# Kernel tuning notes

Measured on AMD Instinct MI355X. Metric: run time of the kernel, lower is better.

## Reference

```python
import jax, jax.numpy as jnp
import numpy as np

HEADS = 8
DIM_HEAD = 64
INNER = HEADS * DIM_HEAD  # 512
QUERY_DIM = 1024
CONTEXT_DIM = 768
OUT_DIM = 1024


def setup_inputs() -> dict:
    key = jax.random.key(0)
    ks = jax.random.split(key, 7)
    B, Nq, Nk = 2, 4096, 4096
    s = 0.02
    return {
        "x": jax.random.normal(ks[0], (B, Nq, QUERY_DIM), dtype=jnp.float32),
        "context": jax.random.normal(ks[1], (B, Nk, CONTEXT_DIM), dtype=jnp.float32),
        "w_q": jax.random.normal(ks[2], (QUERY_DIM, INNER), dtype=jnp.float32) * s,
        "w_k": jax.random.normal(ks[3], (CONTEXT_DIM, INNER), dtype=jnp.float32) * s,
        "w_v": jax.random.normal(ks[4], (CONTEXT_DIM, INNER), dtype=jnp.float32) * s,
        "w_out": jax.random.normal(ks[5], (INNER, OUT_DIM), dtype=jnp.float32) * s,
        "b_out": jax.random.normal(ks[6], (OUT_DIM,), dtype=jnp.float32) * s,
    }


def reference(x, context, w_q, w_k, w_v, w_out, b_out):
    h, d = HEADS, DIM_HEAD
    scale = d ** (-0.5)
    B, Nq, _ = x.shape
    Nk = context.shape[1]
    # projections (no bias)
    q = x @ w_q            # [B, Nq, h*d]
    k = context @ w_k      # [B, Nk, h*d]
    v = context @ w_v      # [B, Nk, h*d]
    # split heads: b n (h d) -> b h n d
    q = q.reshape(B, Nq, h, d).transpose(0, 2, 1, 3)
    k = k.reshape(B, Nk, h, d).transpose(0, 2, 1, 3)
    v = v.reshape(B, Nk, h, d).transpose(0, 2, 1, 3)
    sim = jnp.einsum('bhid,bhjd->bhij', q, k) * scale  # [B, h, Nq, Nk]
    attn = jax.nn.softmax(sim, axis=-1)
    out = jnp.einsum('bhij,bhjd->bhid', attn, v)       # [B, h, Nq, d]
    out = out.transpose(0, 2, 1, 3).reshape(B, Nq, h * d)
    return out @ w_out + b_out  # dropout p=0 -> identity
```

## Files before the change

### kernel.cpp

```cpp
#include <hip/hip_runtime.h>
#include <hip/hip_bf16.h>
#include <stdint.h>

#define HEADS 8
#define DHEAD 64
#define INNER 512
#define QDIM 1024
#define CDIM 768
#define ODIM 1024
#define BATCH 2
#define NQ 4096
#define NKEY 4096

using bf16x8 = __attribute__((ext_vector_type(8))) short;
using f32x4  = __attribute__((ext_vector_type(4))) float;

__device__ __forceinline__ unsigned short f2bf(float x) {
    union { float f; unsigned u; } v; v.f = x;
    unsigned r = v.u + 0x7fffu + ((v.u >> 16) & 1u);
    return (unsigned short)(r >> 16);
}

__device__ __forceinline__ unsigned cvtpk(float a, float b) {
    unsigned r;
    asm("v_cvt_pk_bf16_f32 %0, %1, %2" : "=v"(r) : "v"(a), "v"(b));
    return r;
}

__device__ __forceinline__ float exp2a(float x) {
    float r;
    asm("v_exp_f32 %0, %1" : "=v"(r) : "v"(x));
    return r;
}

typedef const __attribute__((address_space(1))) unsigned int* gptr_t;
typedef __attribute__((address_space(3))) unsigned int* lptr_t;

__device__ __forceinline__ void async16(const void* g, void* l) {
    __builtin_amdgcn_global_load_lds((gptr_t)g, (lptr_t)l, 16, 0, 0);
}

#define SGB __builtin_amdgcn_sched_group_barrier

__global__ void k_convert(const float* __restrict__ in, unsigned short* __restrict__ out, int n4) {
    int i = blockIdx.x * blockDim.x + threadIdx.x;
    int stride = gridDim.x * blockDim.x;
    for (; i < n4; i += stride) {
        float4 v = reinterpret_cast<const float4*>(in)[i];
        ushort4 o;
        o.x = f2bf(v.x); o.y = f2bf(v.y); o.z = f2bf(v.z); o.w = f2bf(v.w);
        reinterpret_cast<ushort4*>(out)[i] = o;
    }
}

__global__ void k_transpose_bf16(const float* __restrict__ in, unsigned short* __restrict__ out,
                                 int R, int C) {
    __shared__ float tile[32][33];
    int c0 = blockIdx.x * 32, r0 = blockIdx.y * 32;
    int tx = threadIdx.x, ty = threadIdx.y;
    #pragma unroll
    for (int i = 0; i < 32; i += 8)
        tile[ty + i][tx] = in[(size_t)(r0 + ty + i) * C + c0 + tx];
    __syncthreads();
    #pragma unroll
    for (int i = 0; i < 32; i += 8)
        out[(size_t)(c0 + ty + i) * R + r0 + tx] = f2bf(tile[tx][ty + i]);
}

template <int OUTMODE>
__global__ __launch_bounds__(256) void k_gemm(const unsigned short* __restrict__ A,
                                              const unsigned short* __restrict__ BT,
                                              void* __restrict__ Cout,
                                              const float* __restrict__ bias,
                                              int M, int N, int Kd, float scale) {
    __shared__ alignas(16) unsigned short As[2][128 * 64];
    __shared__ alignas(16) unsigned short Bs[2][64 * 64];
    const int tid = threadIdx.x, lane = tid & 63, w = tid >> 6;
    const int g = lane >> 4, ql = lane & 15;
    const int m0 = blockIdx.x * 128, n0 = blockIdx.y * 64;
    const int wm = (w >> 1) * 64, wn = (w & 1) * 32;
    f32x4 acc[4][2] = {};

    const int srow = tid >> 3;
    const int schunk = ((tid & 7) ^ (srow & 7)) << 3;
    const unsigned short* gA = A + (size_t)(m0 + srow) * Kd + schunk;
    const unsigned short* gB = BT + (size_t)(n0 + srow) * Kd + schunk;

    auto stage = [&](int buf, int kt) {
        char* lA = (char*)As[buf] + (w << 10);
        char* lB = (char*)Bs[buf] + (w << 10);
        async16(gA + kt, lA);
        async16(gA + kt + (size_t)32 * Kd, lA + 4096);
        async16(gA + kt + (size_t)64 * Kd, lA + 8192);
        async16(gA + kt + (size_t)96 * Kd, lA + 12288);
        async16(gB + kt, lB);
        async16(gB + kt + (size_t)32 * Kd, lB + 4096);
    };

#define GCOMP(BUF) { \
        _Pragma("unroll") \
        for (int kk = 0; kk < 2; kk++) { \
            bf16x8 af[4], bfr[2]; \
            _Pragma("unroll") \
            for (int mi = 0; mi < 4; mi++) { \
                int r = wm + mi * 16 + ql; \
                af[mi] = *(const bf16x8*)((const char*)As[BUF] + r * 128 + ((kk * 64 + (g << 4)) ^ ((r & 7) << 4))); \
            } \
            _Pragma("unroll") \
            for (int ni = 0; ni < 2; ni++) { \
                int r = wn + ni * 16 + ql; \
                bfr[ni] = *(const bf16x8*)((const char*)Bs[BUF] + r * 128 + ((kk * 64 + (g << 4)) ^ ((r & 7) << 4))); \
            } \
            _Pragma("unroll") \
            for (int mi = 0; mi < 4; mi++) \
                _Pragma("unroll") \
                for (int ni = 0; ni < 2; ni++) \
                    acc[mi][ni] = __builtin_amdgcn_mfma_f32_16x16x32_bf16(af[mi], bfr[ni], acc[mi][ni], 0, 0, 0); \
        } \
    }

    stage(0, 0);
    for (int kt = 0; kt < Kd; kt += 128) {
        asm volatile("s_waitcnt vmcnt(0)" ::: "memory");
        __builtin_amdgcn_s_barrier();
        __builtin_amdgcn_sched_barrier(0);
        if (kt + 64 < Kd) stage(1, kt + 64);
        GCOMP(0);
        asm volatile("s_waitcnt vmcnt(0)" ::: "memory");
        __builtin_amdgcn_s_barrier();
        __builtin_amdgcn_sched_barrier(0);
        if (kt + 128 < Kd) stage(0, kt + 128);
        GCOMP(1);
    }
#undef GCOMP

    #pragma unroll
    for (int mi = 0; mi < 4; mi++) {
        #pragma unroll
        for (int ni = 0; ni < 2; ni++) {
            int col = n0 + wn + ni * 16 + ql;
            #pragma unroll
            for (int j = 0; j < 4; j++) {
                int row = m0 + wm + mi * 16 + (g << 2) + j;
                float v = acc[mi][ni][j] * scale;
                if (OUTMODE == 0) {
                    ((unsigned short*)Cout)[(size_t)row * N + col] = f2bf(v);
                } else {
                    ((float*)Cout)[(size_t)row * N + col] = v + bias[col];
                }
            }
        }
    }
}

__global__ __launch_bounds__(256, 2) void k_attn(const unsigned short* __restrict__ Q,
                                                 const unsigned short* __restrict__ K,
                                                 const unsigned short* __restrict__ Vt,
                                                 unsigned short* __restrict__ O) {
    __shared__ alignas(16) unsigned short Ks[2][64 * 64];
    __shared__ alignas(16) unsigned short Vs[2][64 * 64];
    const int tid = threadIdx.x, lane = tid & 63, w = tid >> 6;
    const int g = lane >> 4, ql = lane & 15;
    const int q0 = blockIdx.x * 128;
    const int b = blockIdx.y >> 3, h = blockIdx.y & 7;

    const unsigned short* qp = Q + (size_t)(b * NQ + q0 + w * 32 + ql) * INNER
                                 + h * DHEAD + (g << 3);
    bf16x8 qf00 = *(const bf16x8*)qp;
    bf16x8 qf01 = *(const bf16x8*)(qp + 32);
    bf16x8 qf10 = *(const bf16x8*)(qp + 16 * INNER);
    bf16x8 qf11 = *(const bf16x8*)(qp + 16 * INNER + 32);

    f32x4 po0[4] = {}, po1[4] = {};
    float ls0 = 0.f, ls1 = 0.f;
    const f32x4 zero4 = {0.f, 0.f, 0.f, 0.f};

    const int m0 = tid >> 3;
    const int rho0 = ((m0 & 28) << 1) + (m0 & 3);
    const int srcslot = ((tid & 7) ^ (m0 & 7)) << 3;
    const unsigned short* gK = K + (size_t)(b * NKEY + rho0) * INNER + h * DHEAD + srcslot;
    const unsigned short* gV = Vt + (size_t)(h * DHEAD + m0) * (BATCH * NKEY) + b * NKEY + srcslot;

    auto stageK = [&](int nb, int kt) {
        char* lK = (char*)Ks[nb] + (w << 10);
        async16(gK + (size_t)kt * INNER, lK);
        async16(gK + (size_t)(kt + 4) * INNER, lK + 4096);
    };
    auto stageV = [&](int nb, int kt) {
        char* lV = (char*)Vs[nb] + (w << 10);
        async16(gV + kt, lV);
        async16(gV + kt + (size_t)32 * (BATCH * NKEY), lV + 4096);
    };

    union pfu { bf16x8 v; unsigned u[4]; };

#define SMCHUNK(MI, SC0, SC1, pA, pB, lsa, lsb) { \
        float a0 = exp2a(SC0[MI][0]), a1 = exp2a(SC0[MI][1]); \
        float a2 = exp2a(SC0[MI][2]), a3 = exp2a(SC0[MI][3]); \
        float b0 = exp2a(SC1[MI][0]), b1 = exp2a(SC1[MI][1]); \
        float b2 = exp2a(SC1[MI][2]), b3 = exp2a(SC1[MI][3]); \
        lsa += (a0 + a1) + (a2 + a3); \
        lsb += (b0 + b1) + (b2 + b3); \
        pA[MI & 1].u[(MI >> 1) * 2 + 0] = cvtpk(a0, a1); \
        pA[MI & 1].u[(MI >> 1) * 2 + 1] = cvtpk(a2, a3); \
        pB[MI & 1].u[(MI >> 1) * 2 + 0] = cvtpk(b0, b1); \
        pB[MI & 1].u[(MI >> 1) * 2 + 1] = cvtpk(b2, b3); \
    }

#define QKM(KBUF, S0, S1) { \
        const char* Kb_ = (const char*)(KBUF); \
        _Pragma("unroll") \
        for (int mi = 0; mi < 4; mi++) { \
            int rK = mi * 16 + ql; \
            int sw = (rK & 7) << 4; \
            bf16x8 kf0 = *(const bf16x8*)(Kb_ + rK * 128 + ((g << 4) ^ sw)); \
            bf16x8 kf1 = *(const bf16x8*)(Kb_ + rK * 128 + ((64 + (g << 4)) ^ sw)); \
            S0[mi] = __builtin_amdgcn_mfma_f32_16x16x32_bf16(kf0, qf00, zero4, 0, 0, 0); \
            S0[mi] = __builtin_amdgcn_mfma_f32_16x16x32_bf16(kf1, qf01, S0[mi], 0, 0, 0); \
            S1[mi] = __builtin_amdgcn_mfma_f32_16x16x32_bf16(kf0, qf10, zero4, 0, 0, 0); \
            S1[mi] = __builtin_amdgcn_mfma_f32_16x16x32_bf16(kf1, qf11, S1[mi], 0, 0, 0); \
        } \
    }

#define PVM(VBUF, pA, pB) { \
        const char* Vb_ = (const char*)(VBUF); \
        bf16x8 vf0[4], vf1[4]; \
        _Pragma("unroll") \
        for (int mi = 0; mi < 4; mi++) { \
            int rV = mi * 16 + ql; \
            int sw = (rV & 7) << 4; \
            vf0[mi] = *(const bf16x8*)(Vb_ + rV * 128 + ((g << 4) ^ sw)); \
            vf1[mi] = *(const bf16x8*)(Vb_ + rV * 128 + ((64 + (g << 4)) ^ sw)); \
        } \
        _Pragma("unroll") \
        for (int mi = 0; mi < 4; mi++) { \
            po0[mi] = __builtin_amdgcn_mfma_f32_16x16x32_bf16(vf0[mi], pA[0].v, po0[mi], 0, 0, 0); \
            po0[mi] = __builtin_amdgcn_mfma_f32_16x16x32_bf16(vf1[mi], pA[1].v, po0[mi], 0, 0, 0); \
            po1[mi] = __builtin_amdgcn_mfma_f32_16x16x32_bf16(vf0[mi], pB[0].v, po1[mi], 0, 0, 0); \
            po1[mi] = __builtin_amdgcn_mfma_f32_16x16x32_bf16(vf1[mi], pB[1].v, po1[mi], 0, 0, 0); \
        } \
    }

#define ABODY(T, CUR, SC0, SC1, SN0, SN1, DO_K, DO_V) { \
        asm volatile("s_waitcnt vmcnt(0)" ::: "memory"); \
        __builtin_amdgcn_s_barrier(); \
        __builtin_amdgcn_sched_barrier(0); \
        if (DO_K) stageK(CUR, (T + 2) * 64); \
        if (DO_V) stageV(CUR ^ 1, (T + 1) * 64); \
        const char* Kb_ = (const char*)Ks[CUR ^ 1]; \
        bf16x8 kf0[4], kf1[4]; \
        _Pragma("unroll") \
        for (int mi = 0; mi < 4; mi++) { \
            int rK = mi * 16 + ql; \
            int sw = (rK & 7) << 4; \
            kf0[mi] = *(const bf16x8*)(Kb_ + rK * 128 + ((g << 4) ^ sw)); \
            kf1[mi] = *(const bf16x8*)(Kb_ + rK * 128 + ((64 + (g << 4)) ^ sw)); \
        } \
        __builtin_amdgcn_sched_group_barrier(0x100, 8, 0); \
        pfu pA[2], pB[2]; \
        float lsa = 0.f, lsb = 0.f; \
        _Pragma("unroll") \
        for (int mi = 0; mi < 4; mi++) { \
            SMCHUNK(mi, SC0, SC1, pA, pB, lsa, lsb); \
            __builtin_amdgcn_sched_group_barrier(0x2, 18, 0); \
            SN0[mi] = __builtin_amdgcn_mfma_f32_16x16x32_bf16(kf0[mi], qf00, zero4, 0, 0, 0); \
            SN0[mi] = __builtin_amdgcn_mfma_f32_16x16x32_bf16(kf1[mi], qf01, SN0[mi], 0, 0, 0); \
            SN1[mi] = __builtin_amdgcn_mfma_f32_16x16x32_bf16(kf0[mi], qf10, zero4, 0, 0, 0); \
            SN1[mi] = __builtin_amdgcn_mfma_f32_16x16x32_bf16(kf1[mi], qf11, SN1[mi], 0, 0, 0); \
            __builtin_amdgcn_sched_group_barrier(0x8, 4, 0); \
        } \
        ls0 += lsa; ls1 += lsb; \
        __builtin_amdgcn_s_setprio(1); \
        PVM(Vs[CUR], pA, pB); \
        __builtin_amdgcn_sched_group_barrier(0x100, 8, 0); \
        __builtin_amdgcn_sched_group_barrier(0x8, 16, 0); \
        __builtin_amdgcn_s_setprio(0); \
    }

    f32x4 sE0[4], sE1[4], sO0[4], sO1[4];

    stageK(0, 0); stageV(0, 0); stageK(1, 64);
    asm volatile("s_waitcnt vmcnt(2)" ::: "memory");
    __builtin_amdgcn_s_barrier();
    __builtin_amdgcn_sched_barrier(0);
    QKM(Ks[0], sE0, sE1);

    for (int t = 0; t < 62; t += 2) {
        ABODY(t, 0, sE0, sE1, sO0, sO1, 1, 1);
        ABODY(t + 1, 1, sO0, sO1, sE0, sE1, 1, 1);
    }
    ABODY(62, 0, sE0, sE1, sO0, sO1, 0, 1);

    asm volatile("s_waitcnt vmcnt(0)" ::: "memory");
    __builtin_amdgcn_s_barrier();
    __builtin_amdgcn_sched_barrier(0);
    {
        pfu pA[2], pB[2];
        float lsa = 0.f, lsb = 0.f;
        #pragma unroll
        for (int mi = 0; mi < 4; mi++) {
            SMCHUNK(mi, sO0, sO1, pA, pB, lsa, lsb);
        }
        ls0 += lsa; ls1 += lsb;
        PVM(Vs[1], pA, pB);
    }

    ls0 += __shfl_xor(ls0, 16); ls0 += __shfl_xor(ls0, 32);
    ls1 += __shfl_xor(ls1, 16); ls1 += __shfl_xor(ls1, 32);
    float inv0 = 1.0f / ls0, inv1 = 1.0f / ls1;
    unsigned short* op = O + (size_t)(b * NQ + q0 + w * 32 + ql) * INNER + h * DHEAD + (g << 2);
    #pragma unroll
    for (int mi = 0; mi < 4; mi++) {
        uint2 uu;
        uu.x = cvtpk(po0[mi][0] * inv0, po0[mi][1] * inv0);
        uu.y = cvtpk(po0[mi][2] * inv0, po0[mi][3] * inv0);
        *(uint2*)(op + mi * 16) = uu;
        uint2 vv;
        vv.x = cvtpk(po1[mi][0] * inv1, po1[mi][1] * inv1);
        vv.y = cvtpk(po1[mi][2] * inv1, po1[mi][3] * inv1);
        *(uint2*)(op + 16 * INNER + mi * 16) = vv;
    }
#undef ABODY
#undef PVM
#undef QKM
#undef SMCHUNK
}

extern "C" void kernel_launch(void* const* d_in, const int* in_sizes, int n_in,
                              void* d_out, int out_size, void* d_ws, size_t ws_size,
                              hipStream_t stream) {
    const float* x     = (const float*)d_in[0];
    const float* ctx   = (const float*)d_in[1];
    const float* w_q   = (const float*)d_in[2];
    const float* w_k   = (const float*)d_in[3];
    const float* w_v   = (const float*)d_in[4];
    const float* w_out = (const float*)d_in[5];
    const float* b_out = (const float*)d_in[6];
    float* out = (float*)d_out;

    char* ws = (char*)d_ws;
    size_t off = 0;
    auto alloc = [&](size_t bytes) { void* p = ws + off; off += (bytes + 255) & ~(size_t)255; return p; };
    unsigned short* xb  = (unsigned short*)alloc((size_t)BATCH * NQ * QDIM * 2);
    unsigned short* cb  = (unsigned short*)alloc((size_t)BATCH * NKEY * CDIM * 2);
    unsigned short* wqT = (unsigned short*)alloc((size_t)INNER * QDIM * 2);
    unsigned short* wkT = (unsigned short*)alloc((size_t)INNER * CDIM * 2);
    unsigned short* wvT = (unsigned short*)alloc((size_t)INNER * CDIM * 2);
    unsigned short* woT = (unsigned short*)alloc((size_t)ODIM * INNER * 2);
    unsigned short* Qb  = (unsigned short*)alloc((size_t)BATCH * NQ * INNER * 2);
    unsigned short* Kb  = (unsigned short*)alloc((size_t)BATCH * NKEY * INNER * 2);
    unsigned short* Vtb = (unsigned short*)alloc((size_t)INNER * BATCH * NKEY * 2);
    unsigned short* Ob  = (unsigned short*)alloc((size_t)BATCH * NQ * INNER * 2);

    k_convert<<<2048, 256, 0, stream>>>(x, xb, BATCH * NQ * QDIM / 4);
    k_convert<<<2048, 256, 0, stream>>>(ctx, cb, BATCH * NKEY * CDIM / 4);

    dim3 tb(32, 8);
    k_transpose_bf16<<<dim3(INNER / 32, QDIM / 32), tb, 0, stream>>>(w_q, wqT, QDIM, INNER);
    k_transpose_bf16<<<dim3(INNER / 32, CDIM / 32), tb, 0, stream>>>(w_k, wkT, CDIM, INNER);
    k_transpose_bf16<<<dim3(INNER / 32, CDIM / 32), tb, 0, stream>>>(w_v, wvT, CDIM, INNER);
    k_transpose_bf16<<<dim3(ODIM / 32, INNER / 32), tb, 0, stream>>>(w_out, woT, INNER, ODIM);

    k_gemm<0><<<dim3(8192 / 128, 512 / 64), 256, 0, stream>>>(xb, wqT, Qb, nullptr, 8192, 512, 1024, 0.1803368801111204f);
    k_gemm<0><<<dim3(8192 / 128, 512 / 64), 256, 0, stream>>>(cb, wkT, Kb, nullptr, 8192, 512, 768, 1.0f);
    k_gemm<0><<<dim3(512 / 128, 8192 / 64), 256, 0, stream>>>(wvT, cb, Vtb, nullptr, 512, 8192, 768, 1.0f);

    k_attn<<<dim3(NQ / 128, BATCH * HEADS), 256, 0, stream>>>(Qb, Kb, Vtb, Ob);

    k_gemm<1><<<dim3(8192 / 128, 1024 / 64), 256, 0, stream>>>(Ob, woT, out, b_out, 8192, 1024, 512, 1.0f);
}
```

Before: 156.1 us.

## Split attention over two key halves and merge partials in a combine kernel

The attention kernel gains a third grid dimension that splits the 4096 keys into two halves. Each block writes unnormalized bf16 partial outputs and fp32 row sums, and a new combine kernel adds the two partials and normalizes them. The aim is more blocks per launch for better CU load balance and shorter per-block loops. In exchange it adds a second kernel launch, extra global traffic for the partials, and bf16 rounding of the unnormalized partials. The partial buffers reuse the x and context conversion buffers, which are dead by that point.

```diff
diff --git a/kernel.cpp b/kernel.cpp
--- a/kernel.cpp
+++ b/kernel.cpp
@@ -156,13 +156,20 @@
 __global__ __launch_bounds__(256, 2) void k_attn(const unsigned short* __restrict__ Q,
                                                  const unsigned short* __restrict__ K,
                                                  const unsigned short* __restrict__ Vt,
-                                                 unsigned short* __restrict__ O) {
+                                                 unsigned short* __restrict__ P0,
+                                                 unsigned short* __restrict__ P1,
+                                                 float* __restrict__ L0,
+                                                 float* __restrict__ L1) {
     __shared__ alignas(16) unsigned short Ks[2][64 * 64];
     __shared__ alignas(16) unsigned short Vs[2][64 * 64];
     const int tid = threadIdx.x, lane = tid & 63, w = tid >> 6;
     const int g = lane >> 4, ql = lane & 15;
     const int q0 = blockIdx.x * 128;
     const int b = blockIdx.y >> 3, h = blockIdx.y & 7;
+    const int half = blockIdx.z;
+    const int kbase = half * (NKEY / 2);
+    unsigned short* Pout = half ? P1 : P0;
+    float* Lout = half ? L1 : L0;
 
     const unsigned short* qp = Q + (size_t)(b * NQ + q0 + w * 32 + ql) * INNER
                                  + h * DHEAD + (g << 3);
@@ -178,8 +185,8 @@
     const int m0 = tid >> 3;
     const int rho0 = ((m0 & 28) << 1) + (m0 & 3);
     const int srcslot = ((tid & 7) ^ (m0 & 7)) << 3;
-    const unsigned short* gK = K + (size_t)(b * NKEY + rho0) * INNER + h * DHEAD + srcslot;
-    const unsigned short* gV = Vt + (size_t)(h * DHEAD + m0) * (BATCH * NKEY) + b * NKEY + srcslot;
+    const unsigned short* gK = K + (size_t)(b * NKEY + kbase + rho0) * INNER + h * DHEAD + srcslot;
+    const unsigned short* gV = Vt + (size_t)(h * DHEAD + m0) * (BATCH * NKEY) + b * NKEY + kbase + srcslot;
 
     auto stageK = [&](int nb, int kt) {
         char* lK = (char*)Ks[nb] + (w << 10);
@@ -285,11 +292,11 @@
     __builtin_amdgcn_sched_barrier(0);
     QKM(Ks[0], sE0, sE1);
 
-    for (int t = 0; t < 62; t += 2) {
+    for (int t = 0; t < 30; t += 2) {
         ABODY(t, 0, sE0, sE1, sO0, sO1, 1, 1);
         ABODY(t + 1, 1, sO0, sO1, sE0, sE1, 1, 1);
     }
-    ABODY(62, 0, sE0, sE1, sO0, sO1, 0, 1);
+    ABODY(30, 0, sE0, sE1, sO0, sO1, 0, 1);
 
     asm volatile("s_waitcnt vmcnt(0)" ::: "memory");
     __builtin_amdgcn_s_barrier();
@@ -307,23 +314,51 @@
 
     ls0 += __shfl_xor(ls0, 16); ls0 += __shfl_xor(ls0, 32);
     ls1 += __shfl_xor(ls1, 16); ls1 += __shfl_xor(ls1, 32);
-    float inv0 = 1.0f / ls0, inv1 = 1.0f / ls1;
-    unsigned short* op = O + (size_t)(b * NQ + q0 + w * 32 + ql) * INNER + h * DHEAD + (g << 2);
+    const int row0 = b * NQ + q0 + w * 32 + ql;
+    unsigned short* pp = Pout + (size_t)row0 * INNER + h * DHEAD + (g << 2);
     #pragma unroll
     for (int mi = 0; mi < 4; mi++) {
         uint2 uu;
-        uu.x = cvtpk(po0[mi][0] * inv0, po0[mi][1] * inv0);
-        uu.y = cvtpk(po0[mi][2] * inv0, po0[mi][3] * inv0);
-        *(uint2*)(op + mi * 16) = uu;
+        uu.x = cvtpk(po0[mi][0], po0[mi][1]);
+        uu.y = cvtpk(po0[mi][2], po0[mi][3]);
+        *(uint2*)(pp + mi * 16) = uu;
         uint2 vv;
-        vv.x = cvtpk(po1[mi][0] * inv1, po1[mi][1] * inv1);
-        vv.y = cvtpk(po1[mi][2] * inv1, po1[mi][3] * inv1);
-        *(uint2*)(op + 16 * INNER + mi * 16) = vv;
+        vv.x = cvtpk(po1[mi][0], po1[mi][1]);
+        vv.y = cvtpk(po1[mi][2], po1[mi][3]);
+        *(uint2*)(pp + 16 * INNER + mi * 16) = vv;
+    }
+    if (g == 0) {
+        Lout[(size_t)row0 * HEADS + h] = ls0;
+        Lout[(size_t)(row0 + 16) * HEADS + h] = ls1;
     }
 #undef ABODY
 #undef PVM
 #undef QKM
 #undef SMCHUNK
+}
+
+__global__ __launch_bounds__(256) void k_combine(const unsigned short* __restrict__ P0,
+                                                 const unsigned short* __restrict__ P1,
+                                                 const float* __restrict__ L0,
+                                                 const float* __restrict__ L1,
+                                                 unsigned short* __restrict__ O) {
+    int idx = blockIdx.x * 256 + threadIdx.x;
+    int row = idx >> 6, c8 = idx & 63, h = c8 >> 3;
+    float inv = 1.0f / (L0[(size_t)row * HEADS + h] + L1[(size_t)row * HEADS + h]);
+    uint4 a = ((const uint4*)P0)[idx];
+    uint4 bb = ((const uint4*)P1)[idx];
+    uint4 o;
+    unsigned* ap = (unsigned*)&a;
+    unsigned* bp = (unsigned*)&bb;
+    unsigned* op = (unsigned*)&o;
+    #pragma unroll
+    for (int i = 0; i < 4; i++) {
+        union { unsigned u; float f; } alo, ahi, blo, bhi;
+        alo.u = ap[i] << 16;          ahi.u = ap[i] & 0xffff0000u;
+        blo.u = bp[i] << 16;          bhi.u = bp[i] & 0xffff0000u;
+        op[i] = cvtpk((alo.f + blo.f) * inv, (ahi.f + bhi.f) * inv);
+    }
+    ((uint4*)O)[idx] = o;
 }
 
 extern "C" void kernel_launch(void* const* d_in, const int* in_sizes, int n_in,
@@ -351,6 +386,10 @@
     unsigned short* Kb  = (unsigned short*)alloc((size_t)BATCH * NKEY * INNER * 2);
     unsigned short* Vtb = (unsigned short*)alloc((size_t)INNER * BATCH * NKEY * 2);
     unsigned short* Ob  = (unsigned short*)alloc((size_t)BATCH * NQ * INNER * 2);
+    float* L0 = (float*)alloc((size_t)BATCH * NQ * HEADS * 4);
+    float* L1 = (float*)alloc((size_t)BATCH * NQ * HEADS * 4);
+    unsigned short* P0 = xb;
+    unsigned short* P1 = cb;
 
     k_convert<<<2048, 256, 0, stream>>>(x, xb, BATCH * NQ * QDIM / 4);
     k_convert<<<2048, 256, 0, stream>>>(ctx, cb, BATCH * NKEY * CDIM / 4);
@@ -365,7 +404,8 @@
     k_gemm<0><<<dim3(8192 / 128, 512 / 64), 256, 0, stream>>>(cb, wkT, Kb, nullptr, 8192, 512, 768, 1.0f);
     k_gemm<0><<<dim3(512 / 128, 8192 / 64), 256, 0, stream>>>(wvT, cb, Vtb, nullptr, 512, 8192, 768, 1.0f);
 
-    k_attn<<<dim3(NQ / 128, BATCH * HEADS), 256, 0, stream>>>(Qb, Kb, Vtb, Ob);
+    k_attn<<<dim3(NQ / 128, BATCH * HEADS, 2), 256, 0, stream>>>(Qb, Kb, Vtb, P0, P1, L0, L1);
+    k_combine<<<(BATCH * NQ * INNER / 8) / 256, 256, 0, stream>>>(P0, P1, L0, L1, Ob);
 
     k_gemm<1><<<dim3(8192 / 128, 1024 / 64), 256, 0, stream>>>(Ob, woT, out, b_out, 8192, 1024, 512, 1.0f);
 }
```

Result: slower. 162.3 us (+4.0%).

## Use four-slot K/V ring buffer and barrier every other attention iteration

Applied to the files above, without the earlier changes.

Shared-memory K and V staging grows from double buffering to a four-slot ring. K is now prefetched three tiles ahead and V two tiles ahead. The vmcnt(0) wait plus workgroup barrier runs only on even iterations, which halves synchronization stalls and gives global loads more time in flight. In exchange, LDS use per block doubles to 64KB. The prologue and epilogue are reorganized to match the new slot indexing.

```diff
diff --git a/kernel.cpp b/kernel.cpp
--- a/kernel.cpp
+++ b/kernel.cpp
@@ -157,8 +157,8 @@
                                                  const unsigned short* __restrict__ K,
                                                  const unsigned short* __restrict__ Vt,
                                                  unsigned short* __restrict__ O) {
-    __shared__ alignas(16) unsigned short Ks[2][64 * 64];
-    __shared__ alignas(16) unsigned short Vs[2][64 * 64];
+    __shared__ alignas(16) unsigned short Ks[4][64 * 64];
+    __shared__ alignas(16) unsigned short Vs[4][64 * 64];
     const int tid = threadIdx.x, lane = tid & 63, w = tid >> 6;
     const int g = lane >> 4, ql = lane & 15;
     const int q0 = blockIdx.x * 128;
@@ -181,13 +181,13 @@
     const unsigned short* gK = K + (size_t)(b * NKEY + rho0) * INNER + h * DHEAD + srcslot;
     const unsigned short* gV = Vt + (size_t)(h * DHEAD + m0) * (BATCH * NKEY) + b * NKEY + srcslot;
 
-    auto stageK = [&](int nb, int kt) {
-        char* lK = (char*)Ks[nb] + (w << 10);
+    auto stageK = [&](int slot, int kt) {
+        char* lK = (char*)Ks + (slot << 13) + (w << 10);
         async16(gK + (size_t)kt * INNER, lK);
         async16(gK + (size_t)(kt + 4) * INNER, lK + 4096);
     };
-    auto stageV = [&](int nb, int kt) {
-        char* lV = (char*)Vs[nb] + (w << 10);
+    auto stageV = [&](int slot, int kt) {
+        char* lV = (char*)Vs + (slot << 13) + (w << 10);
         async16(gV + kt, lV);
         async16(gV + kt + (size_t)32 * (BATCH * NKEY), lV + 4096);
     };
@@ -208,13 +208,13 @@
     }
 
 #define QKM(KBUF, S0, S1) { \
-        const char* Kb_ = (const char*)(KBUF); \
+        const char* Kq_ = (const char*)(KBUF); \
         _Pragma("unroll") \
         for (int mi = 0; mi < 4; mi++) { \
             int rK = mi * 16 + ql; \
             int sw = (rK & 7) << 4; \
-            bf16x8 kf0 = *(const bf16x8*)(Kb_ + rK * 128 + ((g << 4) ^ sw)); \
-            bf16x8 kf1 = *(const bf16x8*)(Kb_ + rK * 128 + ((64 + (g << 4)) ^ sw)); \
+            bf16x8 kf0 = *(const bf16x8*)(Kq_ + rK * 128 + ((g << 4) ^ sw)); \
+            bf16x8 kf1 = *(const bf16x8*)(Kq_ + rK * 128 + ((64 + (g << 4)) ^ sw)); \
             S0[mi] = __builtin_amdgcn_mfma_f32_16x16x32_bf16(kf0, qf00, zero4, 0, 0, 0); \
             S0[mi] = __builtin_amdgcn_mfma_f32_16x16x32_bf16(kf1, qf01, S0[mi], 0, 0, 0); \
             S1[mi] = __builtin_amdgcn_mfma_f32_16x16x32_bf16(kf0, qf10, zero4, 0, 0, 0); \
@@ -223,14 +223,14 @@
     }
 
 #define PVM(VBUF, pA, pB) { \
-        const char* Vb_ = (const char*)(VBUF); \
+        const char* Vp_ = (const char*)(VBUF); \
         bf16x8 vf0[4], vf1[4]; \
         _Pragma("unroll") \
         for (int mi = 0; mi < 4; mi++) { \
             int rV = mi * 16 + ql; \
             int sw = (rV & 7) << 4; \
-            vf0[mi] = *(const bf16x8*)(Vb_ + rV * 128 + ((g << 4) ^ sw)); \
-            vf1[mi] = *(const bf16x8*)(Vb_ + rV * 128 + ((64 + (g << 4)) ^ sw)); \
+            vf0[mi] = *(const bf16x8*)(Vp_ + rV * 128 + ((g << 4) ^ sw)); \
+            vf1[mi] = *(const bf16x8*)(Vp_ + rV * 128 + ((64 + (g << 4)) ^ sw)); \
         } \
         _Pragma("unroll") \
         for (int mi = 0; mi < 4; mi++) { \
@@ -241,20 +241,23 @@
         } \
     }
 
-#define ABODY(T, CUR, SC0, SC1, SN0, SN1, DO_K, DO_V) { \
-        asm volatile("s_waitcnt vmcnt(0)" ::: "memory"); \
-        __builtin_amdgcn_s_barrier(); \
-        __builtin_amdgcn_sched_barrier(0); \
-        if (DO_K) stageK(CUR, (T + 2) * 64); \
-        if (DO_V) stageV(CUR ^ 1, (T + 1) * 64); \
-        const char* Kb_ = (const char*)Ks[CUR ^ 1]; \
+#define ABODY(T, BAR, SC0, SC1, SN0, SN1, DO_K, DO_V) { \
+        if (BAR) { \
+            asm volatile("s_waitcnt vmcnt(0)" ::: "memory"); \
+            __builtin_amdgcn_s_barrier(); \
+            __builtin_amdgcn_sched_barrier(0); \
+        } \
+        if (DO_K) stageK(((T) + 3) & 3, ((T) + 3) * 64); \
+        if (DO_V) stageV(((T) + 2) & 3, ((T) + 2) * 64); \
+        const char* Kbase = (const char*)Ks + (((((T) + 1)) & 3) << 13); \
+        const char* Vbase = (const char*)Vs + (((T) & 3) << 13); \
         bf16x8 kf0[4], kf1[4]; \
         _Pragma("unroll") \
         for (int mi = 0; mi < 4; mi++) { \
             int rK = mi * 16 + ql; \
             int sw = (rK & 7) << 4; \
-            kf0[mi] = *(const bf16x8*)(Kb_ + rK * 128 + ((g << 4) ^ sw)); \
-            kf1[mi] = *(const bf16x8*)(Kb_ + rK * 128 + ((64 + (g << 4)) ^ sw)); \
+            kf0[mi] = *(const bf16x8*)(Kbase + rK * 128 + ((g << 4) ^ sw)); \
+            kf1[mi] = *(const bf16x8*)(Kbase + rK * 128 + ((64 + (g << 4)) ^ sw)); \
         } \
         __builtin_amdgcn_sched_group_barrier(0x100, 8, 0); \
         pfu pA[2], pB[2]; \
@@ -271,7 +274,7 @@
         } \
         ls0 += lsa; ls1 += lsb; \
         __builtin_amdgcn_s_setprio(1); \
-        PVM(Vs[CUR], pA, pB); \
+        PVM(Vbase, pA, pB); \
         __builtin_amdgcn_sched_group_barrier(0x100, 8, 0); \
         __builtin_amdgcn_sched_group_barrier(0x8, 16, 0); \
         __builtin_amdgcn_s_setprio(0); \
@@ -279,17 +282,20 @@
 
     f32x4 sE0[4], sE1[4], sO0[4], sO1[4];
 
-    stageK(0, 0); stageV(0, 0); stageK(1, 64);
-    asm volatile("s_waitcnt vmcnt(2)" ::: "memory");
+    stageK(0, 0); stageK(1, 64); stageK(2, 128);
+    stageV(0, 0); stageV(1, 64);
+    asm volatile("s_waitcnt vmcnt(0)" ::: "memory");
     __builtin_amdgcn_s_barrier();
     __builtin_amdgcn_sched_barrier(0);
     QKM(Ks[0], sE0, sE1);
 
-    for (int t = 0; t < 62; t += 2) {
-        ABODY(t, 0, sE0, sE1, sO0, sO1, 1, 1);
-        ABODY(t + 1, 1, sO0, sO1, sE0, sE1, 1, 1);
-    }
-    ABODY(62, 0, sE0, sE1, sO0, sO1, 0, 1);
+    for (int t = 0; t < 60; t += 2) {
+        ABODY(t, 1, sE0, sE1, sO0, sO1, 1, 1);
+        ABODY(t + 1, 0, sO0, sO1, sE0, sE1, 1, 1);
+    }
+    ABODY(60, 1, sE0, sE1, sO0, sO1, 1, 1);
+    ABODY(61, 0, sO0, sO1, sE0, sE1, 0, 1);
+    ABODY(62, 1, sE0, sE1, sO0, sO1, 0, 0);
 
     asm volatile("s_waitcnt vmcnt(0)" ::: "memory");
     __builtin_amdgcn_s_barrier();
@@ -302,7 +308,7 @@
             SMCHUNK(mi, sO0, sO1, pA, pB, lsa, lsb);
         }
         ls0 += lsa; ls1 += lsb;
-        PVM(Vs[1], pA, pB);
+        PVM(Vs[3], pA, pB);
     }
 
     ls0 += __shfl_xor(ls0, 16); ls0 += __shfl_xor(ls0, 32);
```

New measurement: 160.8 us. 3.0% more time.
